# Performance work log

Measured on AMD Instinct MI355X. Metric: run time of the kernel, lower is better.

The kernel has to match this reference:

```python
import jax, jax.numpy as jnp
import numpy as np

NUM_LABELS = 32
PAD_IDX = 0
BS, SEQLEN = 512, 768


def setup_inputs() -> dict:
    key = jax.random.key(0)
    k1, k2, k3, k4, k5 = jax.random.split(key, 5)
    X = jax.random.normal(k1, (BS, SEQLEN, NUM_LABELS), dtype=jnp.float32)
    Y = jax.random.randint(k2, (BS, SEQLEN), 0, NUM_LABELS, dtype=jnp.int32)
    mask = jnp.ones((BS, SEQLEN), dtype=bool)
    # parameters, with the pad-row/col constraints from __init__
    transition = jax.random.normal(k3, (NUM_LABELS, NUM_LABELS), dtype=jnp.float32)
    transition = (transition.at[PAD_IDX, :].set(-10000.0)
                            .at[:, PAD_IDX].set(-10000.0)
                            .at[PAD_IDX, PAD_IDX].set(0.0))
    start_trans = jax.random.normal(k4, (NUM_LABELS,), dtype=jnp.float32).at[PAD_IDX].set(-10000.0)
    end_trans = jax.random.normal(k5, (NUM_LABELS,), dtype=jnp.float32).at[PAD_IDX].set(-10000.0)
    return {"X": X, "Y": Y, "mask": mask, "transition": transition,
            "start_trans": start_trans, "end_trans": end_trans}


def _numerator(X, Y, mask, transition, start_trans, end_trans):
    bs, seqlen, ntag = X.shape
    rb = jnp.arange(bs)
    maskf = mask.astype(X.dtype)
    y0 = Y[:, 0]
    score = start_trans[y0] + X[rb, 0, y0]
    # emissions X[b, t, Y[b,t]] for t>=1, gathered in one shot
    emit = jnp.take_along_axis(X[:, 1:], Y[:, 1:, None], axis=2)[..., 0]  # (bs, seqlen-1)
    tr = transition[Y[:, :-1], Y[:, 1:]]                                   # (bs, seqlen-1)
    score = score + jnp.sum((tr + emit) * maskf[:, 1:], axis=1)
    each_len = jnp.sum(mask, axis=1).astype(jnp.int32)
    last_tag = Y[rb, each_len - 1]
    score = score + end_trans[last_tag] * maskf[rb, each_len - 1]
    return score


def _denominator(X, mask, transition, start_trans, end_trans):
    alpha0 = start_trans + X[:, 0]  # (bs, ntag)

    def step(alpha, xm):
        x_t, m_t = xm  # (bs, ntag), (bs,)
        # logsumexp over previous tag: alpha[b,i] + T[i,j] + x_t[b,j]
        s = alpha[:, :, None] + transition[None, :, :] + x_t[:, None, :]
        new = jax.nn.logsumexp(s, axis=1)
        alpha = jnp.where(m_t[:, None], new, alpha)
        return alpha, None

    xs = (jnp.swapaxes(X[:, 1:], 0, 1), jnp.swapaxes(mask[:, 1:], 0, 1))
    alpha, _ = jax.lax.scan(step, alpha0, xs)
    return jax.nn.logsumexp(alpha + end_trans, axis=1)


def reference(X, Y, mask, transition, start_trans, end_trans):
    log_p = _numerator(X, Y, mask, transition, start_trans, end_trans)
    log_Z = _denominator(X, mask, transition, start_trans, end_trans)
    return log_p - log_Z
```

## Files before the change

kernel.cpp:

```cpp
#include <hip/hip_runtime.h>
#include <hip/hip_bf16.h>

#define NTAG 32
#define SEQLEN 768
#define BS 512
#define NSEG 16
#define SEGLEN 48

typedef __bf16 bf16x8 __attribute__((ext_vector_type(8)));
typedef float f32x16 __attribute__((ext_vector_type(16)));
typedef unsigned u32x4 __attribute__((ext_vector_type(4)));

union BF { bf16x8 v; unsigned u[4]; unsigned short s[8]; };

__device__ __forceinline__ unsigned pk2t(float a, float b) {
  return __builtin_amdgcn_perm(__float_as_uint(b), __float_as_uint(a), 0x07060302u);
}
__device__ __forceinline__ unsigned short trunc1(float a) {
  return (unsigned short)(__float_as_uint(a) >> 16);
}
__device__ __forceinline__ float m3(float a, float b, float c) {
  return fmaxf(fmaxf(a, b), c);
}
__device__ __forceinline__ float max16(const f32x16& a) {
  float g1 = m3(a[0], a[1], a[2]);
  float g2 = m3(a[3], a[4], a[5]);
  float g3 = m3(a[6], a[7], a[8]);
  float g4 = m3(a[9], a[10], a[11]);
  float g5 = m3(a[12], a[13], a[14]);
  return fmaxf(m3(g1, g2, g3), m3(g4, g5, a[15]));
}

#define SEG_STEP(XV, RC) do { \
    float ex_ = __expf(XV) * (RC); \
    u32x4 a1u_, a2u_; \
    _Pragma("unroll") \
    for (int q_ = 0; q_ < 4; ++q_) { \
      a1u_[q_] = pk2t(Eb[2 * q_] * ex_, Eb[2 * q_ + 1] * ex_); \
      a2u_[q_] = pk2t(Eb[8 + 2 * q_] * ex_, Eb[8 + 2 * q_ + 1] * ex_); \
    } \
    acc = __builtin_amdgcn_mfma_f32_32x32x16_bf16( \
        __builtin_bit_cast(bf16x8, a1u_), __builtin_bit_cast(bf16x8, B1u), zf, 0, 0, 0); \
    acc = __builtin_amdgcn_mfma_f32_32x32x16_bf16( \
        __builtin_bit_cast(bf16x8, a2u_), __builtin_bit_cast(bf16x8, B2u), acc, 0, 0, 0); \
    unsigned u0_ = pk2t(acc[0], acc[1]),   u1_ = pk2t(acc[2], acc[3]); \
    unsigned u2_ = pk2t(acc[4], acc[5]),   u3_ = pk2t(acc[6], acc[7]); \
    unsigned u4_ = pk2t(acc[8], acc[9]),   u5_ = pk2t(acc[10], acc[11]); \
    unsigned u6_ = pk2t(acc[12], acc[13]), u7_ = pk2t(acc[14], acc[15]); \
    auto p02_ = __builtin_amdgcn_permlane32_swap(u0_, u2_, false, false); \
    auto p13_ = __builtin_amdgcn_permlane32_swap(u1_, u3_, false, false); \
    auto p46_ = __builtin_amdgcn_permlane32_swap(u4_, u6_, false, false); \
    auto p57_ = __builtin_amdgcn_permlane32_swap(u5_, u7_, false, false); \
    B1u[0] = p02_[0]; B1u[1] = p13_[0]; B1u[2] = p02_[1]; B1u[3] = p13_[1]; \
    B2u[0] = p46_[0]; B2u[1] = p57_[0]; B2u[2] = p46_[1]; B2u[3] = p57_[1]; \
  } while (0)

#define SEG_RESCALE() do { \
    float m_ = max16(acc); \
    m_ = fmaxf(m_, __shfl_xor(m_, 32, 64)); \
    m_ = fmaxf(m_, __shfl_xor(m_, 16, 64)); \
    m_ = fmaxf(m_, __shfl_xor(m_, 8, 64)); \
    m_ = fmaxf(m_, __shfl_xor(m_, 4, 64)); \
    m_ = fmaxf(m_, __shfl_xor(m_, 2, 64)); \
    m_ = fmaxf(m_, __shfl_xor(m_, 1, 64)); \
    c += __logf(m_); \
    rcv = __builtin_amdgcn_rcpf(m_); \
  } while (0)

__global__ __launch_bounds__(256, 4) void crf_seg(
    const float* __restrict__ X, const float* __restrict__ T,
    unsigned short* __restrict__ wsW, float* __restrict__ wsG) {
  const int wid = (blockIdx.x * 256 + threadIdx.x) >> 6;
  const int lane = threadIdx.x & 63;
  const int half = lane >> 5;
  const int r = lane & 31;
  const int b = wid >> 4;
  const int s = wid & (NSEG - 1);
  const int t0 = 1 + s * SEGLEN;

  float Eb[16];
#pragma unroll
  for (int e = 0; e < 8; ++e) {
    Eb[e]     = __expf(T[(8 * half + e) * NTAG + r]);
    Eb[8 + e] = __expf(T[(16 + 8 * half + e) * NTAG + r]);
  }

  u32x4 B1u, B2u;
#pragma unroll
  for (int q = 0; q < 4; ++q) {
    unsigned lo1 = (8 * half + 2 * q == r) ? 0x3F80u : 0u;
    unsigned hi1 = (8 * half + 2 * q + 1 == r) ? 0x3F80u : 0u;
    B1u[q] = lo1 | (hi1 << 16);
    unsigned lo2 = (16 + 8 * half + 2 * q == r) ? 0x3F80u : 0u;
    unsigned hi2 = (16 + 8 * half + 2 * q + 1 == r) ? 0x3F80u : 0u;
    B2u[q] = lo2 | (hi2 << 16);
  }

  const float* xp = X + ((size_t)b * SEQLEN + t0) * NTAG + r;
  f32x16 acc;
  const f32x16 zf = {0.f, 0.f, 0.f, 0.f, 0.f, 0.f, 0.f, 0.f,
                     0.f, 0.f, 0.f, 0.f, 0.f, 0.f, 0.f, 0.f};
  float c = 0.f;
  float rcv = 1.f;

#pragma unroll
  for (int g = 0; g < 11; ++g) {
    float x0 = xp[(size_t)(4 * g + 0) * NTAG];
    float x1 = xp[(size_t)(4 * g + 1) * NTAG];
    float x2 = xp[(size_t)(4 * g + 2) * NTAG];
    float x3 = xp[(size_t)(4 * g + 3) * NTAG];
    SEG_STEP(x0, rcv);
    SEG_STEP(x1, 1.f);
    SEG_STEP(x2, 1.f);
    SEG_STEP(x3, 1.f);
    SEG_RESCALE();
  }
  {
    float x0 = xp[(size_t)44 * NTAG];
    float x1 = xp[(size_t)45 * NTAG];
    float x2 = xp[(size_t)46 * NTAG];
    SEG_STEP(x0, rcv);
    SEG_STEP(x1, 1.f);
    SEG_STEP(x2, 1.f);
    if (s != NSEG - 1) {
      float x3 = xp[(size_t)47 * NTAG];
      SEG_STEP(x3, 1.f);
    }
  }

  float mf = max16(acc);
  mf = fmaxf(mf, __shfl_xor(mf, 32, 64));
  mf = fmaxf(mf, __shfl_xor(mf, 16, 64));
  mf = fmaxf(mf, __shfl_xor(mf, 8, 64));
  mf = fmaxf(mf, __shfl_xor(mf, 4, 64));
  mf = fmaxf(mf, __shfl_xor(mf, 2, 64));
  mf = fmaxf(mf, __shfl_xor(mf, 1, 64));
  float G = c + __logf(mf);
  float sc = __builtin_amdgcn_rcpf(mf);
  unsigned short* W = wsW + ((size_t)wid << 10);
#pragma unroll
  for (int q = 0; q < 4; ++q) {
    uint2 pr;
    pr.x = pk2t(acc[4 * q + 0] * sc, acc[4 * q + 1] * sc);
    pr.y = pk2t(acc[4 * q + 2] * sc, acc[4 * q + 3] * sc);
    *(uint2*)(W + r * NTAG + 8 * q + 4 * half) = pr;
  }
  if (lane == 0) wsG[wid] = G;
}

__device__ __forceinline__ void mat_prod(
    const unsigned short* __restrict__ Wa, const unsigned short* __restrict__ Wb,
    unsigned short* __restrict__ Wd, float ga, float gb, float* __restrict__ gd,
    int lane) {
  const int half = lane >> 5;
  const int r = lane & 31;
  BF A1, A2, Bf1, Bf2;
  A1.v = *(const bf16x8*)(Wa + r * NTAG + 8 * half);
  A2.v = *(const bf16x8*)(Wa + r * NTAG + 16 + 8 * half);
#pragma unroll
  for (int e = 0; e < 8; ++e) {
    Bf1.s[e] = Wb[(8 * half + e) * NTAG + r];
    Bf2.s[e] = Wb[(16 + 8 * half + e) * NTAG + r];
  }
  const f32x16 zf = {0.f, 0.f, 0.f, 0.f, 0.f, 0.f, 0.f, 0.f,
                     0.f, 0.f, 0.f, 0.f, 0.f, 0.f, 0.f, 0.f};
  f32x16 d = __builtin_amdgcn_mfma_f32_32x32x16_bf16(A1.v, Bf1.v, zf, 0, 0, 0);
  d = __builtin_amdgcn_mfma_f32_32x32x16_bf16(A2.v, Bf2.v, d, 0, 0, 0);
  float m = max16(d);
  m = fmaxf(m, __shfl_xor(m, 32, 64));
  m = fmaxf(m, __shfl_xor(m, 16, 64));
  m = fmaxf(m, __shfl_xor(m, 8, 64));
  m = fmaxf(m, __shfl_xor(m, 4, 64));
  m = fmaxf(m, __shfl_xor(m, 2, 64));
  m = fmaxf(m, __shfl_xor(m, 1, 64));
  m = fmaxf(m, 1e-35f);
  float sc = __builtin_amdgcn_rcpf(m);
#pragma unroll
  for (int reg = 0; reg < 16; ++reg) {
    int row = (reg & 3) + 8 * (reg >> 2) + 4 * half;
    Wd[row * NTAG + r] = trunc1(d[reg] * sc);
  }
  if (lane == 0) *gd = ga + gb + __logf(m);
}

__global__ __launch_bounds__(256) void crf_tree(
    const float* __restrict__ X, const int* __restrict__ Y,
    const float* __restrict__ transition, const float* __restrict__ start_trans,
    const float* __restrict__ end_trans,
    const unsigned short* __restrict__ wsW, const float* __restrict__ wsG,
    float* __restrict__ out) {
  __shared__ unsigned short Wl[16][NTAG * NTAG];
  __shared__ unsigned short Wn[8][NTAG * NTAG];
  __shared__ float Ga[16], Gb[8];
  __shared__ float red[4];
  const int b = blockIdx.x;
  const int tid = threadIdx.x;
  const int w = tid >> 6;
  const int lane = tid & 63;
  const int half = lane >> 5;
  const int r = lane & 31;
  const float* Xb = X + (size_t)b * (SEQLEN * NTAG);
  const int* Yb = Y + (size_t)b * SEQLEN;

  {
    const uint4* s4 = (const uint4*)(wsW + ((size_t)b << 14));
    uint4* d4 = (uint4*)&Wl[0][0];
#pragma unroll
    for (int i = 0; i < 8; ++i) d4[tid + 256 * i] = s4[tid + 256 * i];
  }
  if (tid < 16) Ga[tid] = wsG[b * 16 + tid];

  float ns = 0.f;
#pragma unroll
  for (int it = 0; it < 3; ++it) {
    int t = 1 + tid + it * 256;
    if (t < SEQLEN) {
      int yp = Yb[t - 1];
      int yc = Yb[t];
      ns += transition[yp * NTAG + yc] + Xb[t * NTAG + yc];
    }
  }
  if (tid == 0) {
    int y0 = Yb[0];
    int ylast = Yb[SEQLEN - 1];
    ns += start_trans[y0] + Xb[y0] + end_trans[ylast];
  }
  ns += __shfl_xor(ns, 32, 64);
  ns += __shfl_xor(ns, 16, 64);
  ns += __shfl_xor(ns, 8, 64);
  ns += __shfl_xor(ns, 4, 64);
  ns += __shfl_xor(ns, 2, 64);
  ns += __shfl_xor(ns, 1, 64);
  if (lane == 0) red[w] = ns;
  __syncthreads();

  mat_prod(Wl[2 * w], Wl[2 * w + 1], Wn[w], Ga[2 * w], Ga[2 * w + 1], &Gb[w], lane);
  mat_prod(Wl[2 * (w + 4)], Wl[2 * (w + 4) + 1], Wn[w + 4],
           Ga[2 * (w + 4)], Ga[2 * (w + 4) + 1], &Gb[w + 4], lane);
  __syncthreads();
  mat_prod(Wn[2 * w], Wn[2 * w + 1], Wl[w], Gb[2 * w], Gb[2 * w + 1], &Ga[w], lane);
  __syncthreads();
  if (w < 2)
    mat_prod(Wl[2 * w], Wl[2 * w + 1], Wn[w], Ga[2 * w], Ga[2 * w + 1], &Gb[w], lane);
  __syncthreads();
  if (w == 0) {
    BF A1, A2, Bf1, Bf2;
    A1.v = *(const bf16x8*)(&Wn[0][0] + r * NTAG + 8 * half);
    A2.v = *(const bf16x8*)(&Wn[0][0] + r * NTAG + 16 + 8 * half);
#pragma unroll
    for (int e = 0; e < 8; ++e) {
      Bf1.s[e] = Wn[1][(8 * half + e) * NTAG + r];
      Bf2.s[e] = Wn[1][(16 + 8 * half + e) * NTAG + r];
    }
    const f32x16 zf = {0.f, 0.f, 0.f, 0.f, 0.f, 0.f, 0.f, 0.f,
                       0.f, 0.f, 0.f, 0.f, 0.f, 0.f, 0.f, 0.f};
    f32x16 d = __builtin_amdgcn_mfma_f32_32x32x16_bf16(A1.v, Bf1.v, zf, 0, 0, 0);
    d = __builtin_amdgcn_mfma_f32_32x32x16_bf16(A2.v, Bf2.v, d, 0, 0, 0);

    float a0 = start_trans[r] + Xb[r];
    float m0 = a0;
    m0 = fmaxf(m0, __shfl_xor(m0, 16, 32));
    m0 = fmaxf(m0, __shfl_xor(m0, 8, 32));
    m0 = fmaxf(m0, __shfl_xor(m0, 4, 32));
    m0 = fmaxf(m0, __shfl_xor(m0, 2, 32));
    m0 = fmaxf(m0, __shfl_xor(m0, 1, 32));
    float p = __expf(a0 - m0);
    float zsum = 0.f;
#pragma unroll
    for (int reg = 0; reg < 16; ++reg) {
      int row = (reg & 3) + 8 * (reg >> 2) + 4 * half;
      zsum = fmaf(__shfl(p, row, 32), d[reg], zsum);
    }
    float t = zsum * __expf(end_trans[r]);
    t += __shfl_xor(t, 32, 64);
    t += __shfl_xor(t, 16, 64);
    t += __shfl_xor(t, 8, 64);
    t += __shfl_xor(t, 4, 64);
    t += __shfl_xor(t, 2, 64);
    t += __shfl_xor(t, 1, 64);
    t = fmaxf(t, 1e-35f);
    if (lane == 0) {
      float numer = red[0] + red[1] + red[2] + red[3];
      out[b] = numer - (m0 + Gb[0] + Gb[1] + __logf(t));
    }
  }
}

extern "C" void kernel_launch(void* const* d_in, const int* in_sizes, int n_in,
                              void* d_out, int out_size, void* d_ws, size_t ws_size,
                              hipStream_t stream) {
  const float* X = (const float*)d_in[0];
  const int* Y = (const int*)d_in[1];
  const float* transition = (const float*)d_in[3];
  const float* start_trans = (const float*)d_in[4];
  const float* end_trans = (const float*)d_in[5];
  float* out = (float*)d_out;

  unsigned short* wsW = (unsigned short*)d_ws;
  float* wsG = (float*)((char*)d_ws + (size_t)BS * NSEG * (NTAG * NTAG * 2));

  crf_seg<<<(BS * NSEG) / 4, 256, 0, stream>>>(X, transition, wsW, wsG);
  crf_tree<<<BS, 256, 0, stream>>>(X, Y, transition, start_trans, end_trans,
                                   wsW, wsG, out);
}
```

Baseline: 61.18 us.

## Switch segment scan to fp16 MFMA with packed exp-transition multiply and 2-step rescale

Converts the bf16 MFMA pipeline to fp16: transition exponentials are prepacked as half2, so each step scales them by exp(x) with packed f16 multiplies instead of eight fp32 multiplies plus truncation packing. The per-step rescale factor is folded into the exponent argument (cadd), using a fixed log(1/64) offset to keep values within fp16 range. Rescaling now happens every 2 steps instead of every 4, and the x loads are software-prefetched one iteration ahead in a non-unrolled loop. The cost is fp16's narrower dynamic range, which brings a risk of overflow or underflow, plus more frequent reductions.

New measurement: 59.14 us. 3.3% less time.

```diff
diff --git a/kernel.cpp b/kernel.cpp
--- a/kernel.cpp
+++ b/kernel.cpp
@@ -7,17 +7,21 @@
 #define NSEG 16
 #define SEGLEN 48
 
-typedef __bf16 bf16x8 __attribute__((ext_vector_type(8)));
+typedef _Float16 f16x2 __attribute__((ext_vector_type(2)));
+typedef _Float16 f16x8 __attribute__((ext_vector_type(8)));
 typedef float f32x16 __attribute__((ext_vector_type(16)));
 typedef unsigned u32x4 __attribute__((ext_vector_type(4)));
 
-union BF { bf16x8 v; unsigned u[4]; unsigned short s[8]; };
-
-__device__ __forceinline__ unsigned pk2t(float a, float b) {
-  return __builtin_amdgcn_perm(__float_as_uint(b), __float_as_uint(a), 0x07060302u);
-}
-__device__ __forceinline__ unsigned short trunc1(float a) {
-  return (unsigned short)(__float_as_uint(a) >> 16);
+union HF { f16x8 v; unsigned u[4]; unsigned short s[8]; };
+
+#define MEXP6 (-4.15888308f)
+
+__device__ __forceinline__ unsigned short trunch(float a) {
+  return __builtin_bit_cast(unsigned short, (_Float16)a);
+}
+__device__ __forceinline__ unsigned pkh(float a, float b) {
+  auto t = __builtin_amdgcn_cvt_pkrtz(a, b);
+  return __builtin_bit_cast(unsigned, t);
 }
 __device__ __forceinline__ float m3(float a, float b, float c) {
   return fmaxf(fmaxf(a, b), c);
@@ -31,22 +35,24 @@
   return fmaxf(m3(g1, g2, g3), m3(g4, g5, a[15]));
 }
 
-#define SEG_STEP(XV, RC) do { \
-    float ex_ = __expf(XV) * (RC); \
-    u32x4 a1u_, a2u_; \
+#define SEG_STEP(XV, CADD) do { \
+    float ex_ = __expf((XV) + (CADD)); \
+    unsigned exw_ = pkh(ex_, ex_); \
+    f16x2 exx_ = __builtin_bit_cast(f16x2, exw_); \
+    u32x4 a1w_, a2w_; \
     _Pragma("unroll") \
     for (int q_ = 0; q_ < 4; ++q_) { \
-      a1u_[q_] = pk2t(Eb[2 * q_] * ex_, Eb[2 * q_ + 1] * ex_); \
-      a2u_[q_] = pk2t(Eb[8 + 2 * q_] * ex_, Eb[8 + 2 * q_ + 1] * ex_); \
+      a1w_[q_] = __builtin_bit_cast(unsigned, (f16x2)(__builtin_bit_cast(f16x2, Ep1[q_]) * exx_)); \
+      a2w_[q_] = __builtin_bit_cast(unsigned, (f16x2)(__builtin_bit_cast(f16x2, Ep2[q_]) * exx_)); \
     } \
-    acc = __builtin_amdgcn_mfma_f32_32x32x16_bf16( \
-        __builtin_bit_cast(bf16x8, a1u_), __builtin_bit_cast(bf16x8, B1u), zf, 0, 0, 0); \
-    acc = __builtin_amdgcn_mfma_f32_32x32x16_bf16( \
-        __builtin_bit_cast(bf16x8, a2u_), __builtin_bit_cast(bf16x8, B2u), acc, 0, 0, 0); \
-    unsigned u0_ = pk2t(acc[0], acc[1]),   u1_ = pk2t(acc[2], acc[3]); \
-    unsigned u2_ = pk2t(acc[4], acc[5]),   u3_ = pk2t(acc[6], acc[7]); \
-    unsigned u4_ = pk2t(acc[8], acc[9]),   u5_ = pk2t(acc[10], acc[11]); \
-    unsigned u6_ = pk2t(acc[12], acc[13]), u7_ = pk2t(acc[14], acc[15]); \
+    acc = __builtin_amdgcn_mfma_f32_32x32x16_f16( \
+        __builtin_bit_cast(f16x8, a1w_), __builtin_bit_cast(f16x8, B1u), zf, 0, 0, 0); \
+    acc = __builtin_amdgcn_mfma_f32_32x32x16_f16( \
+        __builtin_bit_cast(f16x8, a2w_), __builtin_bit_cast(f16x8, B2u), acc, 0, 0, 0); \
+    unsigned u0_ = pkh(acc[0], acc[1]),   u1_ = pkh(acc[2], acc[3]); \
+    unsigned u2_ = pkh(acc[4], acc[5]),   u3_ = pkh(acc[6], acc[7]); \
+    unsigned u4_ = pkh(acc[8], acc[9]),   u5_ = pkh(acc[10], acc[11]); \
+    unsigned u6_ = pkh(acc[12], acc[13]), u7_ = pkh(acc[14], acc[15]); \
     auto p02_ = __builtin_amdgcn_permlane32_swap(u0_, u2_, false, false); \
     auto p13_ = __builtin_amdgcn_permlane32_swap(u1_, u3_, false, false); \
     auto p46_ = __builtin_amdgcn_permlane32_swap(u4_, u6_, false, false); \
@@ -63,8 +69,10 @@
     m_ = fmaxf(m_, __shfl_xor(m_, 4, 64)); \
     m_ = fmaxf(m_, __shfl_xor(m_, 2, 64)); \
     m_ = fmaxf(m_, __shfl_xor(m_, 1, 64)); \
-    c += __logf(m_); \
-    rcv = __builtin_amdgcn_rcpf(m_); \
+    m_ = fmaxf(m_, 1e-30f); \
+    float lg_ = __logf(m_); \
+    c += lg_; \
+    cadd = MEXP6 - lg_; \
   } while (0)
 
 __global__ __launch_bounds__(256, 4) void crf_seg(
@@ -78,55 +86,56 @@
   const int s = wid & (NSEG - 1);
   const int t0 = 1 + s * SEGLEN;
 
-  float Eb[16];
-#pragma unroll
-  for (int e = 0; e < 8; ++e) {
-    Eb[e]     = __expf(T[(8 * half + e) * NTAG + r]);
-    Eb[8 + e] = __expf(T[(16 + 8 * half + e) * NTAG + r]);
+  u32x4 Ep1, Ep2;
+#pragma unroll
+  for (int q = 0; q < 4; ++q) {
+    float e0 = __expf(T[(8 * half + 2 * q) * NTAG + r]);
+    float e1 = __expf(T[(8 * half + 2 * q + 1) * NTAG + r]);
+    float e2 = __expf(T[(16 + 8 * half + 2 * q) * NTAG + r]);
+    float e3 = __expf(T[(16 + 8 * half + 2 * q + 1) * NTAG + r]);
+    Ep1[q] = pkh(e0, e1);
+    Ep2[q] = pkh(e2, e3);
   }
 
   u32x4 B1u, B2u;
 #pragma unroll
   for (int q = 0; q < 4; ++q) {
-    unsigned lo1 = (8 * half + 2 * q == r) ? 0x3F80u : 0u;
-    unsigned hi1 = (8 * half + 2 * q + 1 == r) ? 0x3F80u : 0u;
+    unsigned lo1 = (8 * half + 2 * q == r) ? 0x3C00u : 0u;
+    unsigned hi1 = (8 * half + 2 * q + 1 == r) ? 0x3C00u : 0u;
     B1u[q] = lo1 | (hi1 << 16);
-    unsigned lo2 = (16 + 8 * half + 2 * q == r) ? 0x3F80u : 0u;
-    unsigned hi2 = (16 + 8 * half + 2 * q + 1 == r) ? 0x3F80u : 0u;
+    unsigned lo2 = (16 + 8 * half + 2 * q == r) ? 0x3C00u : 0u;
+    unsigned hi2 = (16 + 8 * half + 2 * q + 1 == r) ? 0x3C00u : 0u;
     B2u[q] = lo2 | (hi2 << 16);
   }
 
-  const float* xp = X + ((size_t)b * SEQLEN + t0) * NTAG + r;
+  const float* xw = X + ((size_t)b * SEQLEN + t0) * NTAG + r;
   f32x16 acc;
   const f32x16 zf = {0.f, 0.f, 0.f, 0.f, 0.f, 0.f, 0.f, 0.f,
                      0.f, 0.f, 0.f, 0.f, 0.f, 0.f, 0.f, 0.f};
   float c = 0.f;
-  float rcv = 1.f;
-
-#pragma unroll
-  for (int g = 0; g < 11; ++g) {
-    float x0 = xp[(size_t)(4 * g + 0) * NTAG];
-    float x1 = xp[(size_t)(4 * g + 1) * NTAG];
-    float x2 = xp[(size_t)(4 * g + 2) * NTAG];
-    float x3 = xp[(size_t)(4 * g + 3) * NTAG];
-    SEG_STEP(x0, rcv);
-    SEG_STEP(x1, 1.f);
-    SEG_STEP(x2, 1.f);
-    SEG_STEP(x3, 1.f);
+  float cadd = MEXP6;
+
+  float x0 = xw[0];
+  float x1 = xw[NTAG];
+
+  for (int w = 0; w < 22; ++w) {
+    float n0 = xw[(size_t)(2 * w + 2) * NTAG];
+    float n1 = xw[(size_t)(2 * w + 3) * NTAG];
+    SEG_STEP(x0, cadd);
+    SEG_STEP(x1, MEXP6);
     SEG_RESCALE();
+    x0 = n0; x1 = n1;
   }
   {
-    float x0 = xp[(size_t)44 * NTAG];
-    float x1 = xp[(size_t)45 * NTAG];
-    float x2 = xp[(size_t)46 * NTAG];
-    SEG_STEP(x0, rcv);
-    SEG_STEP(x1, 1.f);
-    SEG_STEP(x2, 1.f);
-    if (s != NSEG - 1) {
-      float x3 = xp[(size_t)47 * NTAG];
-      SEG_STEP(x3, 1.f);
-    }
-  }
+    float n0 = xw[(size_t)46 * NTAG];
+    float n1 = xw[(size_t)(s == NSEG - 1 ? 46 : 47) * NTAG];
+    SEG_STEP(x0, cadd);
+    SEG_STEP(x1, MEXP6);
+    SEG_RESCALE();
+    x0 = n0; x1 = n1;
+  }
+  SEG_STEP(x0, cadd);
+  if (s != NSEG - 1) SEG_STEP(x1, MEXP6);
 
   float mf = max16(acc);
   mf = fmaxf(mf, __shfl_xor(mf, 32, 64));
@@ -135,14 +144,15 @@
   mf = fmaxf(mf, __shfl_xor(mf, 4, 64));
   mf = fmaxf(mf, __shfl_xor(mf, 2, 64));
   mf = fmaxf(mf, __shfl_xor(mf, 1, 64));
+  mf = fmaxf(mf, 1e-30f);
   float G = c + __logf(mf);
   float sc = __builtin_amdgcn_rcpf(mf);
   unsigned short* W = wsW + ((size_t)wid << 10);
 #pragma unroll
   for (int q = 0; q < 4; ++q) {
     uint2 pr;
-    pr.x = pk2t(acc[4 * q + 0] * sc, acc[4 * q + 1] * sc);
-    pr.y = pk2t(acc[4 * q + 2] * sc, acc[4 * q + 3] * sc);
+    pr.x = pkh(acc[4 * q + 0] * sc, acc[4 * q + 1] * sc);
+    pr.y = pkh(acc[4 * q + 2] * sc, acc[4 * q + 3] * sc);
     *(uint2*)(W + r * NTAG + 8 * q + 4 * half) = pr;
   }
   if (lane == 0) wsG[wid] = G;
@@ -154,9 +164,9 @@
     int lane) {
   const int half = lane >> 5;
   const int r = lane & 31;
-  BF A1, A2, Bf1, Bf2;
-  A1.v = *(const bf16x8*)(Wa + r * NTAG + 8 * half);
-  A2.v = *(const bf16x8*)(Wa + r * NTAG + 16 + 8 * half);
+  HF A1, A2, Bf1, Bf2;
+  A1.v = *(const f16x8*)(Wa + r * NTAG + 8 * half);
+  A2.v = *(const f16x8*)(Wa + r * NTAG + 16 + 8 * half);
 #pragma unroll
   for (int e = 0; e < 8; ++e) {
     Bf1.s[e] = Wb[(8 * half + e) * NTAG + r];
@@ -164,8 +174,8 @@
   }
   const f32x16 zf = {0.f, 0.f, 0.f, 0.f, 0.f, 0.f, 0.f, 0.f,
                      0.f, 0.f, 0.f, 0.f, 0.f, 0.f, 0.f, 0.f};
-  f32x16 d = __builtin_amdgcn_mfma_f32_32x32x16_bf16(A1.v, Bf1.v, zf, 0, 0, 0);
-  d = __builtin_amdgcn_mfma_f32_32x32x16_bf16(A2.v, Bf2.v, d, 0, 0, 0);
+  f32x16 d = __builtin_amdgcn_mfma_f32_32x32x16_f16(A1.v, Bf1.v, zf, 0, 0, 0);
+  d = __builtin_amdgcn_mfma_f32_32x32x16_f16(A2.v, Bf2.v, d, 0, 0, 0);
   float m = max16(d);
   m = fmaxf(m, __shfl_xor(m, 32, 64));
   m = fmaxf(m, __shfl_xor(m, 16, 64));
@@ -173,12 +183,12 @@
   m = fmaxf(m, __shfl_xor(m, 4, 64));
   m = fmaxf(m, __shfl_xor(m, 2, 64));
   m = fmaxf(m, __shfl_xor(m, 1, 64));
-  m = fmaxf(m, 1e-35f);
+  m = fmaxf(m, 1e-30f);
   float sc = __builtin_amdgcn_rcpf(m);
 #pragma unroll
   for (int reg = 0; reg < 16; ++reg) {
     int row = (reg & 3) + 8 * (reg >> 2) + 4 * half;
-    Wd[row * NTAG + r] = trunc1(d[reg] * sc);
+    Wd[row * NTAG + r] = trunch(d[reg] * sc);
   }
   if (lane == 0) *gd = ga + gb + __logf(m);
 }
@@ -244,9 +254,9 @@
     mat_prod(Wl[2 * w], Wl[2 * w + 1], Wn[w], Ga[2 * w], Ga[2 * w + 1], &Gb[w], lane);
   __syncthreads();
   if (w == 0) {
-    BF A1, A2, Bf1, Bf2;
-    A1.v = *(const bf16x8*)(&Wn[0][0] + r * NTAG + 8 * half);
-    A2.v = *(const bf16x8*)(&Wn[0][0] + r * NTAG + 16 + 8 * half);
+    HF A1, A2, Bf1, Bf2;
+    A1.v = *(const f16x8*)(&Wn[0][0] + r * NTAG + 8 * half);
+    A2.v = *(const f16x8*)(&Wn[0][0] + r * NTAG + 16 + 8 * half);
 #pragma unroll
     for (int e = 0; e < 8; ++e) {
       Bf1.s[e] = Wn[1][(8 * half + e) * NTAG + r];
@@ -254,8 +264,8 @@
     }
     const f32x16 zf = {0.f, 0.f, 0.f, 0.f, 0.f, 0.f, 0.f, 0.f,
                        0.f, 0.f, 0.f, 0.f, 0.f, 0.f, 0.f, 0.f};
-    f32x16 d = __builtin_amdgcn_mfma_f32_32x32x16_bf16(A1.v, Bf1.v, zf, 0, 0, 0);
-    d = __builtin_amdgcn_mfma_f32_32x32x16_bf16(A2.v, Bf2.v, d, 0, 0, 0);
+    f32x16 d = __builtin_amdgcn_mfma_f32_32x32x16_f16(A1.v, Bf1.v, zf, 0, 0, 0);
+    d = __builtin_amdgcn_mfma_f32_32x32x16_f16(A2.v, Bf2.v, d, 0, 0, 0);
 
     float a0 = start_trans[r] + Xb[r];
     float m0 = a0;
```
